# Optimization experiments

Measured on AMD Instinct MI355X. Metric: run time of the kernel, lower is better.

## Reference

```python
import jax, jax.numpy as jnp
import numpy as np

B, T, C, NH = 4, 2048, 1024, 16
HD = C // NH  # head dim = 64


def setup_inputs() -> dict:
    key = jax.random.key(0)
    k1, k2, k3 = jax.random.split(key, 3)
    x = jax.random.normal(k1, (B, T, C), dtype=jnp.float32)
    w_attn = jax.random.normal(k2, (C, 3 * C), dtype=jnp.float32) * (1.0 / np.sqrt(C))
    b_attn = jnp.zeros((3 * C,), dtype=jnp.float32)
    w_proj = jax.random.normal(k3, (C, C), dtype=jnp.float32) * (1.0 / np.sqrt(C))
    b_proj = jnp.zeros((C,), dtype=jnp.float32)
    return {"x": x, "w_attn": w_attn, "b_attn": b_attn, "w_proj": w_proj, "b_proj": b_proj}


def reference(x, w_attn, b_attn, w_proj, b_proj):
    Bx, Tx, Cx = x.shape
    # fused QKV projection
    qkv = x @ w_attn + b_attn              # [B, T, 3C]
    q, k, v = jnp.split(qkv, 3, axis=-1)   # each [B, T, C]
    # split heads: [B, NH, T, HD]
    q = q.reshape(Bx, Tx, NH, HD).transpose(0, 2, 1, 3)
    k = k.reshape(Bx, Tx, NH, HD).transpose(0, 2, 1, 3)
    v = v.reshape(Bx, Tx, NH, HD).transpose(0, 2, 1, 3)
    scale = 1.0 / np.sqrt(HD)
    att = jnp.einsum('bhqd,bhkd->bhqk', q, k) * scale  # [B, NH, T, T]
    causal = jnp.tril(jnp.ones((Tx, Tx), dtype=bool))
    att = jnp.where(causal[None, None], att, -jnp.inf)
    att = jax.nn.softmax(att, axis=-1)
    y = jnp.einsum('bhqk,bhkd->bhqd', att, v)           # [B, NH, T, HD]
    y = y.transpose(0, 2, 1, 3).reshape(Bx, Tx, Cx)
    return y @ w_proj + b_proj
```

## Files before the change

### kernel.cpp

```cpp
#include <hip/hip_runtime.h>
#include <hip/hip_bf16.h>

#define B_SZ 4
#define T_SZ 2048
#define C_SZ 1024
#define NH_SZ 16
#define HD_SZ 64
#define M_SZ (B_SZ * T_SZ)

typedef __bf16 bf16x8 __attribute__((ext_vector_type(8)));
typedef __bf16 bf16x4 __attribute__((ext_vector_type(4)));
typedef float f32x4 __attribute__((ext_vector_type(4)));

__device__ __forceinline__ void async_ld16(__hip_bfloat16* lds, const __hip_bfloat16* g) {
  __builtin_amdgcn_global_load_lds(
      (const __attribute__((address_space(1))) void*)g,
      (__attribute__((address_space(3))) void*)lds, 16, 0, 0);
}

__device__ __forceinline__ void bar() {
  asm volatile("" ::: "memory");
  __builtin_amdgcn_s_barrier();
  asm volatile("" ::: "memory");
}

__device__ __forceinline__ bf16x8 frag32(const __hip_bfloat16* base, int row, int q) {
  const int byte = (row << 6) + (((q ^ (row >> 1)) & 3) << 4);
  return *(const bf16x8*)((const char*)base + byte);
}

__global__ __launch_bounds__(256) void conv_bf16_kernel(
    const float* __restrict__ X, __hip_bfloat16* __restrict__ Y) {
  const int i = (blockIdx.x * 256 + threadIdx.x) * 4;
  float4 v = *(const float4*)&X[i];
  union { bf16x4 v; __hip_bfloat16 h[4]; } o;
  o.h[0] = __float2bfloat16(v.x); o.h[1] = __float2bfloat16(v.y);
  o.h[2] = __float2bfloat16(v.z); o.h[3] = __float2bfloat16(v.w);
  *(bf16x4*)&Y[i] = o.v;
}

template <int KD, int ND>
__global__ __launch_bounds__(256) void transpose_conv_kernel(
    const float* __restrict__ W, __hip_bfloat16* __restrict__ Wt) {
  __shared__ float sT[32][33];
  const int n0 = blockIdx.x * 32, k0 = blockIdx.y * 32;
  const int tid = threadIdx.x;
  {
    const int r = tid >> 3, c = (tid & 7) * 4;
    float4 v = *(const float4*)&W[(size_t)(k0 + r) * ND + n0 + c];
    sT[r][c] = v.x; sT[r][c + 1] = v.y; sT[r][c + 2] = v.z; sT[r][c + 3] = v.w;
  }
  __syncthreads();
  {
    const int n = tid >> 3, kq = (tid & 7) * 4;
    union { bf16x4 v; __hip_bfloat16 h[4]; } o;
#pragma unroll
    for (int j = 0; j < 4; ++j) o.h[j] = __float2bfloat16(sT[kq + j][n]);
    *(bf16x4*)&Wt[(size_t)(n0 + n) * KD + k0 + kq] = o.v;
  }
}


__global__ __launch_bounds__(512, 2) void gemm_tri256_qk(
    const __hip_bfloat16* __restrict__ A, const __hip_bfloat16* __restrict__ Bt,
    const float* __restrict__ bias,
    __hip_bfloat16* __restrict__ qR, __hip_bfloat16* __restrict__ kR) {
  __shared__ __align__(16) __hip_bfloat16 sA[3][256 * 32];
  __shared__ __align__(16) __hip_bfloat16 sB[3][256 * 32];

  const int tid = threadIdx.x;
  const int wave = tid >> 6, lane = tid & 63;
  const int quad = lane >> 4, l16 = lane & 15;
  const int wm = wave >> 2, wn = wave & 3;

  const int xcd = (int)blockIdx.x & 7, lb = (int)blockIdx.x >> 3;
  const int bm = (xcd * 4 + (lb >> 3)) * 256;
  const int bn = (lb & 7) * 256;

  const int srow = tid >> 2;
  const int scol = 8 * ((tid & 3) ^ ((tid >> 3) & 3));
  const int sdst = tid * 8;
  const __hip_bfloat16* gA = A + (size_t)(bm + srow) * C_SZ + scol;
  const __hip_bfloat16* gB = Bt + (size_t)(bn + srow) * C_SZ + scol;

  f32x4 acc[8][4];
#pragma unroll
  for (int m = 0; m < 8; ++m)
#pragma unroll
    for (int n = 0; n < 4; ++n) acc[m][n] = (f32x4){0.f, 0.f, 0.f, 0.f};

#define STG256(buf, kt)                                                         \
  do {                                                                          \
    async_ld16(&sA[buf][sdst], gA + (kt) * 32);                                 \
    async_ld16(&sA[buf][4096 + sdst], gA + (size_t)128 * C_SZ + (kt) * 32);     \
    async_ld16(&sB[buf][sdst], gB + (kt) * 32);                                 \
    async_ld16(&sB[buf][4096 + sdst], gB + (size_t)128 * C_SZ + (kt) * 32);     \
  } while (0)

  STG256(0, 0);
  STG256(1, 1);
  asm volatile("s_waitcnt vmcnt(4)" ::: "memory");
  bar();

  constexpr int NT = C_SZ / 32;
  int cur = 0;
  for (int kt = 0; kt < NT; ++kt) {
    const int stg = cur == 0 ? 2 : cur - 1;
    if (kt + 2 < NT) STG256(stg, kt + 2);

    const __hip_bfloat16* ab = sA[cur];
    const __hip_bfloat16* bb = sB[cur];
    bf16x8 af[8], bfr[4];
#pragma unroll
    for (int mq = 0; mq < 8; ++mq) af[mq] = frag32(ab, wm * 128 + mq * 16 + l16, quad);
#pragma unroll
    for (int nq = 0; nq < 4; ++nq) bfr[nq] = frag32(bb, wn * 64 + nq * 16 + l16, quad);
#pragma unroll
    for (int mq = 0; mq < 8; ++mq)
#pragma unroll
      for (int nq = 0; nq < 4; ++nq)
        acc[mq][nq] = __builtin_amdgcn_mfma_f32_16x16x32_bf16(af[mq], bfr[nq], acc[mq][nq], 0, 0, 0);

    if (kt + 1 < NT) {
      if (kt + 2 < NT) asm volatile("s_waitcnt vmcnt(4)" ::: "memory");
      else             asm volatile("s_waitcnt vmcnt(0)" ::: "memory");
      bar();
    }
    cur = cur == 2 ? 0 : cur + 1;
  }
#undef STG256

  float bv[4];
#pragma unroll
  for (int nq = 0; nq < 4; ++nq) bv[nq] = bias[bn + wn * 64 + nq * 16 + l16];
  const bool isQ = bn < C_SZ;
#pragma unroll
  for (int mq = 0; mq < 8; ++mq)
#pragma unroll
    for (int nq = 0; nq < 4; ++nq) {
      const int col = bn + wn * 64 + nq * 16 + l16;
      const int hh = (col >> 6) & 15, d = col & 63;
#pragma unroll
      for (int r = 0; r < 4; ++r) {
        const int row = bm + wm * 128 + mq * 16 + quad * 4 + r;
        const int bb_ = row >> 11, t = row & 2047;
        const size_t idx = ((size_t)(bb_ * 16 + hh) * T_SZ + t) * HD_SZ + d;
        const float val = acc[mq][nq][r] + bv[nq];
        if (isQ) qR[idx] = __float2bfloat16(val * 0.125f);
        else     kR[idx] = __float2bfloat16(val);
      }
    }
}

template <int MODE>
__global__ __launch_bounds__(256, 3) void gemm_tri128(
    const __hip_bfloat16* __restrict__ A, const __hip_bfloat16* __restrict__ Bt,
    const float* __restrict__ bias, float* __restrict__ Cf,
    __hip_bfloat16* __restrict__ vT) {
  __shared__ __align__(16) __hip_bfloat16 sA[3][128 * 32];
  __shared__ __align__(16) __hip_bfloat16 sB[3][128 * 32];

  const int tid = threadIdx.x;
  const int wave = tid >> 6, lane = tid & 63;
  const int quad = lane >> 4, l16 = lane & 15;
  const int rw = (wave & 1) * 64, cw = (wave >> 1) * 64;

  const int xcd = (int)blockIdx.x & 7, lb = (int)blockIdx.x >> 3;
  const int bm = (xcd * 8 + (lb >> 3)) * 128;
  const int bn = (lb & 7) * 128;

  const int srow = tid >> 2;
  const int scol = 8 * ((tid & 3) ^ ((tid >> 3) & 3));
  const int sdst = tid * 8;
  const __hip_bfloat16* gA = A + (size_t)(bm + srow) * C_SZ + scol;
  const __hip_bfloat16* gB = Bt + (size_t)(bn + srow) * C_SZ + scol;

  f32x4 acc[4][4];
#pragma unroll
  for (int i = 0; i < 4; ++i)
#pragma unroll
    for (int j = 0; j < 4; ++j) acc[i][j] = (f32x4){0.f, 0.f, 0.f, 0.f};

#define STG128(buf, kt)                                                        \
  do {                                                                         \
    async_ld16(&sA[buf][sdst], gA + (kt) * 32);                                \
    async_ld16(&sA[buf][2048 + sdst], gA + (size_t)64 * C_SZ + (kt) * 32);     \
    async_ld16(&sB[buf][sdst], gB + (kt) * 32);                                \
    async_ld16(&sB[buf][2048 + sdst], gB + (size_t)64 * C_SZ + (kt) * 32);     \
  } while (0)

  STG128(0, 0);
  STG128(1, 1);
  asm volatile("s_waitcnt vmcnt(4)" ::: "memory");
  bar();

  constexpr int NT = C_SZ / 32;
  int cur = 0;
  for (int kt = 0; kt < NT; ++kt) {
    const int stg = cur == 0 ? 2 : cur - 1;
    if (kt + 2 < NT) STG128(stg, kt + 2);

    const __hip_bfloat16* ab = sA[cur];
    const __hip_bfloat16* bb = sB[cur];
    bf16x8 af[4], bfr[4];
#pragma unroll
    for (int mq = 0; mq < 4; ++mq) af[mq] = frag32(ab, rw + mq * 16 + l16, quad);
#pragma unroll
    for (int nq = 0; nq < 4; ++nq) bfr[nq] = frag32(bb, cw + nq * 16 + l16, quad);
#pragma unroll
    for (int mq = 0; mq < 4; ++mq)
#pragma unroll
      for (int nq = 0; nq < 4; ++nq)
        acc[mq][nq] = __builtin_amdgcn_mfma_f32_16x16x32_bf16(af[mq], bfr[nq], acc[mq][nq], 0, 0, 0);

    if (kt + 1 < NT) {
      if (kt + 2 < NT) asm volatile("s_waitcnt vmcnt(4)" ::: "memory");
      else             asm volatile("s_waitcnt vmcnt(0)" ::: "memory");
      bar();
    }
    cur = cur == 2 ? 0 : cur + 1;
  }
#undef STG128

  float bv[4];
#pragma unroll
  for (int nq = 0; nq < 4; ++nq) bv[nq] = bias[bn + cw + nq * 16 + l16];
#pragma unroll
  for (int mq = 0; mq < 4; ++mq)
#pragma unroll
    for (int nq = 0; nq < 4; ++nq) {
      const int col = bn + cw + nq * 16 + l16;
#pragma unroll
      for (int r = 0; r < 4; ++r) {
        const int row = bm + rw + mq * 16 + quad * 4 + r;
        const float val = acc[mq][nq][r] + bv[nq];
        if (MODE == 0) {
          const int bb_ = row >> 11, t = row & 2047;
          const int hh = col >> 6, d = col & 63;
          vT[((size_t)(bb_ * 16 + hh) * HD_SZ + d) * T_SZ + t] = __float2bfloat16(val);
        } else {
          Cf[(size_t)row * C_SZ + col] = val;
        }
      }
    }
}

#define ATT_ST 72

__global__ __launch_bounds__(256, 4) void attn_mfma_kernel(
    const __hip_bfloat16* __restrict__ qR, const __hip_bfloat16* __restrict__ kR,
    const __hip_bfloat16* __restrict__ vT, __hip_bfloat16* __restrict__ y) {
  __shared__ __align__(16) __hip_bfloat16 sQ[64][ATT_ST];
  __shared__ __align__(16) __hip_bfloat16 sK[64][ATT_ST];
  __shared__ __align__(16) __hip_bfloat16 sVt[64][ATT_ST];
  __shared__ __align__(16) __hip_bfloat16 sP[64][ATT_ST];

  const int bh = blockIdx.x;
  const int tile = (int)gridDim.y - 1 - blockIdx.y;
  const int t0 = tile * 64;
  const int tid = threadIdx.x;
  const int wave = tid >> 6, lane = tid & 63;
  const int quad = lane >> 4, l16 = lane & 15;
  const int wrow0 = wave * 16;

  const __hip_bfloat16* qb = qR + (size_t)bh * T_SZ * HD_SZ;
  const __hip_bfloat16* kb = kR + (size_t)bh * T_SZ * HD_SZ;
  const __hip_bfloat16* vb = vT + (size_t)bh * HD_SZ * T_SZ;

  const int sr = tid >> 2, sc = (tid & 3) * 16;

  {
    const __hip_bfloat16* src = qb + (size_t)t0 * HD_SZ + tid * 16;
    *(float4*)&sQ[sr][sc] = *(const float4*)src;
    *(float4*)&sQ[sr][sc + 8] = *(const float4*)(src + 8);
  }

  float4 krg0, krg1, vrg0, vrg1;
  {
    const __hip_bfloat16* ks = kb + tid * 16;
    krg0 = *(const float4*)ks;
    krg1 = *(const float4*)(ks + 8);
    const __hip_bfloat16* vs = vb + (size_t)sr * T_SZ + sc;
    vrg0 = *(const float4*)vs;
    vrg1 = *(const float4*)(vs + 8);
  }

  __syncthreads();
  bf16x8 qa0 = *(const bf16x8*)&sQ[wrow0 + l16][quad * 8];
  bf16x8 qa1 = *(const bf16x8*)&sQ[wrow0 + l16][32 + quad * 8];

  float lp[4];
  f32x4 o[4];
#pragma unroll
  for (int r = 0; r < 4; ++r) lp[r] = 0.f;
#pragma unroll
  for (int nn = 0; nn < 4; ++nn) o[nn] = (f32x4){0.f, 0.f, 0.f, 0.f};

  for (int j0 = 0; j0 <= t0; j0 += 64) {
    *(float4*)&sK[sr][sc] = krg0;
    *(float4*)&sK[sr][sc + 8] = krg1;
    *(float4*)&sVt[sr][sc] = vrg0;
    *(float4*)&sVt[sr][sc + 8] = vrg1;
    if (j0 + 64 <= t0) {
      const __hip_bfloat16* ks = kb + (size_t)(j0 + 64) * HD_SZ + tid * 16;
      krg0 = *(const float4*)ks;
      krg1 = *(const float4*)(ks + 8);
      const __hip_bfloat16* vs = vb + (size_t)sr * T_SZ + j0 + 64 + sc;
      vrg0 = *(const float4*)vs;
      vrg1 = *(const float4*)(vs + 8);
    }
    __syncthreads();

    f32x4 s[4];
#pragma unroll
    for (int sub = 0; sub < 4; ++sub) {
      s[sub] = (f32x4){0.f, 0.f, 0.f, 0.f};
      bf16x8 kf0 = *(const bf16x8*)&sK[sub * 16 + l16][quad * 8];
      s[sub] = __builtin_amdgcn_mfma_f32_16x16x32_bf16(qa0, kf0, s[sub], 0, 0, 0);
      bf16x8 kf1 = *(const bf16x8*)&sK[sub * 16 + l16][32 + quad * 8];
      s[sub] = __builtin_amdgcn_mfma_f32_16x16x32_bf16(qa1, kf1, s[sub], 0, 0, 0);
    }

    if (j0 == t0) {
#pragma unroll
      for (int sub = 0; sub < 4; ++sub) {
        const int key_l = sub * 16 + l16;
#pragma unroll
        for (int r = 0; r < 4; ++r) {
          const int row_l = wrow0 + quad * 4 + r;
          if (key_l > row_l) s[sub][r] = -1e30f;
        }
      }
    }

#pragma unroll
    for (int sub = 0; sub < 4; ++sub)
#pragma unroll
      for (int r = 0; r < 4; ++r) s[sub][r] = __expf(s[sub][r]);
#pragma unroll
    for (int r = 0; r < 4; ++r)
      lp[r] += (s[0][r] + s[1][r]) + (s[2][r] + s[3][r]);

#pragma unroll
    for (int sub = 0; sub < 4; ++sub)
#pragma unroll
      for (int r = 0; r < 4; ++r)
        sP[wrow0 + quad * 4 + r][sub * 16 + l16] = __float2bfloat16(s[sub][r]);

    bf16x8 pa0 = *(const bf16x8*)&sP[wrow0 + l16][quad * 8];
    bf16x8 pa1 = *(const bf16x8*)&sP[wrow0 + l16][32 + quad * 8];

#pragma unroll
    for (int nn = 0; nn < 4; ++nn) {
      bf16x8 vf0 = *(const bf16x8*)&sVt[nn * 16 + l16][quad * 8];
      o[nn] = __builtin_amdgcn_mfma_f32_16x16x32_bf16(pa0, vf0, o[nn], 0, 0, 0);
      bf16x8 vf1 = *(const bf16x8*)&sVt[nn * 16 + l16][32 + quad * 8];
      o[nn] = __builtin_amdgcn_mfma_f32_16x16x32_bf16(pa1, vf1, o[nn], 0, 0, 0);
    }

    if (j0 < t0) __syncthreads();
  }

#pragma unroll
  for (int off = 1; off <= 8; off <<= 1)
#pragma unroll
    for (int r = 0; r < 4; ++r) lp[r] += __shfl_xor(lp[r], off);
  float inv[4];
#pragma unroll
  for (int r = 0; r < 4; ++r) inv[r] = 1.0f / lp[r];

  const int b = bh >> 4, h = bh & 15;
#pragma unroll
  for (int nn = 0; nn < 4; ++nn)
#pragma unroll
    for (int r = 0; r < 4; ++r) {
      const int t = t0 + wrow0 + quad * 4 + r;
      y[((size_t)b * T_SZ + t) * C_SZ + h * HD_SZ + nn * 16 + l16] =
          __float2bfloat16(o[nn][r] * inv[r]);
    }
}

extern "C" void kernel_launch(void* const* d_in, const int* in_sizes, int n_in,
                              void* d_out, int out_size, void* d_ws, size_t ws_size,
                              hipStream_t stream) {
  const float* x      = (const float*)d_in[0];
  const float* w_attn = (const float*)d_in[1];
  const float* b_attn = (const float*)d_in[2];
  const float* w_proj = (const float*)d_in[3];
  const float* b_proj = (const float*)d_in[4];
  float* out = (float*)d_out;

  __hip_bfloat16* xb  = (__hip_bfloat16*)d_ws;
  __hip_bfloat16* waT = xb + (size_t)M_SZ * C_SZ;
  __hip_bfloat16* wpT = waT + (size_t)3 * C_SZ * C_SZ;
  __hip_bfloat16* qR  = wpT + (size_t)C_SZ * C_SZ;
  __hip_bfloat16* kR  = qR + (size_t)M_SZ * C_SZ;
  __hip_bfloat16* vT  = kR + (size_t)M_SZ * C_SZ;
  __hip_bfloat16* yb  = xb;

  conv_bf16_kernel<<<(M_SZ * C_SZ) / (256 * 4), 256, 0, stream>>>(x, xb);
  transpose_conv_kernel<C_SZ, 3 * C_SZ><<<dim3(96, 32), 256, 0, stream>>>(w_attn, waT);
  transpose_conv_kernel<C_SZ, C_SZ><<<dim3(32, 32), 256, 0, stream>>>(w_proj, wpT);

  gemm_tri256_qk<<<dim3(256), 512, 0, stream>>>(xb, waT, b_attn, qR, kR);

  gemm_tri128<0><<<dim3(512), 256, 0, stream>>>(
      xb, waT + (size_t)2 * C_SZ * C_SZ, b_attn + 2 * C_SZ, nullptr, vT);

  attn_mfma_kernel<<<dim3(B_SZ * NH_SZ, T_SZ / 64), 256, 0, stream>>>(qR, kR, vT, yb);

  gemm_tri128<1><<<dim3(512), 256, 0, stream>>>(
      (const __hip_bfloat16*)yb, wpT, b_proj, out, nullptr);
}
```

Before: 265.2 us.

## Keep attention probabilities in registers via transposed QK MFMA and lane shuffles

The attention kernel now computes S transposed by swapping the MFMA operands, so each lane holds scores for one query row. It then packs the exponentiated probabilities into bf16 pairs and redistributes them with cross-lane shuffles into the A-operand layout for the PV MFMA, dropping the sP shared-memory round trip and its LDS traffic. The Q prescale now folds in log2(e) so the kernel can use the hardware exp2 instead of __expf. Row sums are accumulated per lane and reduced at the end with fewer shuffles, at the cost of extra shuffle and select instructions inside the loop.

```diff
diff --git a/kernel.cpp b/kernel.cpp
--- a/kernel.cpp
+++ b/kernel.cpp
@@ -27,6 +27,13 @@
 __device__ __forceinline__ bf16x8 frag32(const __hip_bfloat16* base, int row, int q) {
   const int byte = (row << 6) + (((q ^ (row >> 1)) & 3) << 4);
   return *(const bf16x8*)((const char*)base + byte);
+}
+
+__device__ __forceinline__ uint32_t pk2(float lo, float hi) {
+  union { __hip_bfloat16 h; unsigned short u; } a, b;
+  a.h = __float2bfloat16(lo);
+  b.h = __float2bfloat16(hi);
+  return (uint32_t)a.u | ((uint32_t)b.u << 16);
 }
 
 __global__ __launch_bounds__(256) void conv_bf16_kernel(
@@ -61,6 +68,8 @@
 }
 
 
+#define Q_PRESCALE 0.18033688011112042f
+
 __global__ __launch_bounds__(512, 2) void gemm_tri256_qk(
     const __hip_bfloat16* __restrict__ A, const __hip_bfloat16* __restrict__ Bt,
     const float* __restrict__ bias,
@@ -146,7 +155,7 @@
         const int bb_ = row >> 11, t = row & 2047;
         const size_t idx = ((size_t)(bb_ * 16 + hh) * T_SZ + t) * HD_SZ + d;
         const float val = acc[mq][nq][r] + bv[nq];
-        if (isQ) qR[idx] = __float2bfloat16(val * 0.125f);
+        if (isQ) qR[idx] = __float2bfloat16(val * Q_PRESCALE);
         else     kR[idx] = __float2bfloat16(val);
       }
     }
@@ -253,7 +262,6 @@
   __shared__ __align__(16) __hip_bfloat16 sQ[64][ATT_ST];
   __shared__ __align__(16) __hip_bfloat16 sK[64][ATT_ST];
   __shared__ __align__(16) __hip_bfloat16 sVt[64][ATT_ST];
-  __shared__ __align__(16) __hip_bfloat16 sP[64][ATT_ST];
 
   const int bh = blockIdx.x;
   const int tile = (int)gridDim.y - 1 - blockIdx.y;
@@ -268,6 +276,11 @@
   const __hip_bfloat16* vb = vT + (size_t)bh * HD_SZ * T_SZ;
 
   const int sr = tid >> 2, sc = (tid & 3) * 16;
+
+  const bool uSel = (quad & 1) != 0;
+  const bool cSel = (quad >> 1) != 0;
+  const int srcE = l16 + 32 * (quad & 1) + 16 * (quad >> 1);
+  const int srcO = srcE ^ 16;
 
   {
     const __hip_bfloat16* src = qb + (size_t)t0 * HD_SZ + tid * 16;
@@ -289,10 +302,8 @@
   bf16x8 qa0 = *(const bf16x8*)&sQ[wrow0 + l16][quad * 8];
   bf16x8 qa1 = *(const bf16x8*)&sQ[wrow0 + l16][32 + quad * 8];
 
-  float lp[4];
+  float lacc = 0.f;
   f32x4 o[4];
-#pragma unroll
-  for (int r = 0; r < 4; ++r) lp[r] = 0.f;
 #pragma unroll
   for (int nn = 0; nn < 4; ++nn) o[nn] = (f32x4){0.f, 0.f, 0.f, 0.f};
 
@@ -316,58 +327,68 @@
     for (int sub = 0; sub < 4; ++sub) {
       s[sub] = (f32x4){0.f, 0.f, 0.f, 0.f};
       bf16x8 kf0 = *(const bf16x8*)&sK[sub * 16 + l16][quad * 8];
-      s[sub] = __builtin_amdgcn_mfma_f32_16x16x32_bf16(qa0, kf0, s[sub], 0, 0, 0);
+      s[sub] = __builtin_amdgcn_mfma_f32_16x16x32_bf16(kf0, qa0, s[sub], 0, 0, 0);
       bf16x8 kf1 = *(const bf16x8*)&sK[sub * 16 + l16][32 + quad * 8];
-      s[sub] = __builtin_amdgcn_mfma_f32_16x16x32_bf16(qa1, kf1, s[sub], 0, 0, 0);
+      s[sub] = __builtin_amdgcn_mfma_f32_16x16x32_bf16(kf1, qa1, s[sub], 0, 0, 0);
     }
 
     if (j0 == t0) {
-#pragma unroll
-      for (int sub = 0; sub < 4; ++sub) {
-        const int key_l = sub * 16 + l16;
-#pragma unroll
-        for (int r = 0; r < 4; ++r) {
-          const int row_l = wrow0 + quad * 4 + r;
-          if (key_l > row_l) s[sub][r] = -1e30f;
-        }
-      }
+      const int qrow = wrow0 + l16;
+#pragma unroll
+      for (int sub = 0; sub < 4; ++sub)
+#pragma unroll
+        for (int r = 0; r < 4; ++r)
+          if (sub * 16 + quad * 4 + r > qrow) s[sub][r] = -1e30f;
     }
 
 #pragma unroll
     for (int sub = 0; sub < 4; ++sub)
 #pragma unroll
-      for (int r = 0; r < 4; ++r) s[sub][r] = __expf(s[sub][r]);
-#pragma unroll
-    for (int r = 0; r < 4; ++r)
-      lp[r] += (s[0][r] + s[1][r]) + (s[2][r] + s[3][r]);
-
+      for (int r = 0; r < 4; ++r) s[sub][r] = __builtin_amdgcn_exp2f(s[sub][r]);
 #pragma unroll
     for (int sub = 0; sub < 4; ++sub)
-#pragma unroll
-      for (int r = 0; r < 4; ++r)
-        sP[wrow0 + quad * 4 + r][sub * 16 + l16] = __float2bfloat16(s[sub][r]);
-
-    bf16x8 pa0 = *(const bf16x8*)&sP[wrow0 + l16][quad * 8];
-    bf16x8 pa1 = *(const bf16x8*)&sP[wrow0 + l16][32 + quad * 8];
+      lacc += (s[sub][0] + s[sub][1]) + (s[sub][2] + s[sub][3]);
+
+    uint32_t pk[4][2];
+#pragma unroll
+    for (int sub = 0; sub < 4; ++sub)
+#pragma unroll
+      for (int h = 0; h < 2; ++h)
+        pk[sub][h] = pk2(s[sub][2 * h], s[sub][2 * h + 1]);
+
+    uint32_t g0 = (uint32_t)__shfl((int)(uSel ? pk[1][0] : pk[0][0]), srcE, 64);
+    uint32_t g1 = (uint32_t)__shfl((int)(uSel ? pk[0][0] : pk[1][0]), srcO, 64);
+    uint32_t g2 = (uint32_t)__shfl((int)(uSel ? pk[3][0] : pk[2][0]), srcE, 64);
+    uint32_t g3 = (uint32_t)__shfl((int)(uSel ? pk[2][0] : pk[3][0]), srcO, 64);
+    uint32_t g4 = (uint32_t)__shfl((int)(uSel ? pk[1][1] : pk[0][1]), srcE, 64);
+    uint32_t g5 = (uint32_t)__shfl((int)(uSel ? pk[0][1] : pk[1][1]), srcO, 64);
+    uint32_t g6 = (uint32_t)__shfl((int)(uSel ? pk[3][1] : pk[2][1]), srcE, 64);
+    uint32_t g7 = (uint32_t)__shfl((int)(uSel ? pk[2][1] : pk[3][1]), srcO, 64);
+
+    union PU { uint32_t d[4]; bf16x8 v; };
+    PU A0, A1;
+    A0.d[0] = cSel ? g1 : g0;  A0.d[1] = cSel ? g5 : g4;
+    A0.d[2] = cSel ? g0 : g1;  A0.d[3] = cSel ? g4 : g5;
+    A1.d[0] = cSel ? g3 : g2;  A1.d[1] = cSel ? g7 : g6;
+    A1.d[2] = cSel ? g2 : g3;  A1.d[3] = cSel ? g6 : g7;
 
 #pragma unroll
     for (int nn = 0; nn < 4; ++nn) {
       bf16x8 vf0 = *(const bf16x8*)&sVt[nn * 16 + l16][quad * 8];
-      o[nn] = __builtin_amdgcn_mfma_f32_16x16x32_bf16(pa0, vf0, o[nn], 0, 0, 0);
+      o[nn] = __builtin_amdgcn_mfma_f32_16x16x32_bf16(A0.v, vf0, o[nn], 0, 0, 0);
       bf16x8 vf1 = *(const bf16x8*)&sVt[nn * 16 + l16][32 + quad * 8];
-      o[nn] = __builtin_amdgcn_mfma_f32_16x16x32_bf16(pa1, vf1, o[nn], 0, 0, 0);
+      o[nn] = __builtin_amdgcn_mfma_f32_16x16x32_bf16(A1.v, vf1, o[nn], 0, 0, 0);
     }
 
     if (j0 < t0) __syncthreads();
   }
 
-#pragma unroll
-  for (int off = 1; off <= 8; off <<= 1)
-#pragma unroll
-    for (int r = 0; r < 4; ++r) lp[r] += __shfl_xor(lp[r], off);
+  lacc += __shfl_xor(lacc, 16);
+  lacc += __shfl_xor(lacc, 32);
   float inv[4];
 #pragma unroll
-  for (int r = 0; r < 4; ++r) inv[r] = 1.0f / lp[r];
+  for (int r = 0; r < 4; ++r)
+    inv[r] = 1.0f / __shfl(lacc, (lane & 48) + quad * 4 + r, 64);
 
   const int b = bh >> 4, h = bh & 15;
 #pragma unroll
```

Result: faster. 257.3 us (-3.0%).
